# Kernel tuning notes

Measured on AMD Instinct MI355X. Metric: run time of the kernel, lower is better.

Reference implementation:

```python
import jax, jax.numpy as jnp
import numpy as np

N = 50000
E = 800000
F_IN = 512
H = 128
K = 10
ALPHA = 0.1
EPS = 1e-5  # BatchNorm eps


def setup_inputs() -> dict:
    key = jax.random.key(0)
    ks = jax.random.split(key, 16)
    x = jax.random.normal(ks[0], (N, F_IN), dtype=jnp.float32)
    edge_index = jax.random.randint(ks[1], (2, E), 0, N, dtype=jnp.int64)
    # Linear weights (xavier-ish scale)
    W1 = jax.random.normal(ks[2], (F_IN, H), dtype=jnp.float32) * (1.0 / np.sqrt(F_IN))
    b1 = jnp.zeros((H,), dtype=jnp.float32)
    W2 = jax.random.normal(ks[3], (H, H), dtype=jnp.float32) * (1.0 / np.sqrt(H))
    b2 = jnp.zeros((H,), dtype=jnp.float32)
    # BatchNorm (eval mode: running stats)
    gamma1 = jnp.ones((H,), dtype=jnp.float32)
    beta1 = jnp.zeros((H,), dtype=jnp.float32)
    mean1 = jax.random.normal(ks[4], (H,), dtype=jnp.float32) * 0.1
    var1 = jax.random.uniform(ks[5], (H,), dtype=jnp.float32) + 0.5
    gamma2 = jnp.ones((H,), dtype=jnp.float32)
    beta2 = jnp.zeros((H,), dtype=jnp.float32)
    mean2 = jax.random.normal(ks[6], (H,), dtype=jnp.float32) * 0.1
    var2 = jax.random.uniform(ks[7], (H,), dtype=jnp.float32) + 0.5
    return {
        "x": x, "edge_index": edge_index,
        "W1": W1, "b1": b1, "gamma1": gamma1, "beta1": beta1, "mean1": mean1, "var1": var1,
        "W2": W2, "b2": b2, "gamma2": gamma2, "beta2": beta2, "mean2": mean2, "var2": var2,
    }


def _bn_eval(h, gamma, beta, mean, var):
    return (h - mean) * jax.lax.rsqrt(var + EPS) * gamma + beta


def _appnp_prop(h, edge_index):
    # add self loops
    loop = jnp.arange(N, dtype=edge_index.dtype)
    src = jnp.concatenate([edge_index[0], loop])
    dst = jnp.concatenate([edge_index[1], loop])
    # symmetric GCN normalization: deg^{-1/2}[src] * deg^{-1/2}[dst]
    deg = jax.ops.segment_sum(jnp.ones_like(src, dtype=h.dtype), dst, num_segments=N)
    dinv = jax.lax.rsqrt(jnp.maximum(deg, 1.0))
    norm = dinv[src] * dinv[dst]  # [E+N]
    h0 = h

    def step(carry, _):
        msg = carry[src] * norm[:, None]                    # [E+N, H]
        agg = jax.ops.segment_sum(msg, dst, num_segments=N)  # [N, H]
        return (1.0 - ALPHA) * agg + ALPHA * h0, None

    out, _ = jax.lax.scan(step, h, None, length=K)
    return out


def reference(x, edge_index, W1, b1, gamma1, beta1, mean1, var1,
              W2, b2, gamma2, beta2, mean2, var2):
    h = jax.nn.relu(x @ W1 + b1)
    h = _bn_eval(h, gamma1, beta1, mean1, var1)
    # dropout inactive (eval mode)
    h = h @ W2 + b2
    h = _bn_eval(h, gamma2, beta2, mean2, var2)
    return _appnp_prop(h, edge_index)
```

## Files before the change

### kernel.cpp

```cpp
#include <hip/hip_runtime.h>

#define ALPHA_F 0.1f
#define EPS_F   1e-5f

typedef float    f32x4 __attribute__((ext_vector_type(4)));
typedef _Float16 h16x8 __attribute__((ext_vector_type(8)));
typedef _Float16 h16x2 __attribute__((ext_vector_type(2)));

__device__ __forceinline__ void gll16(const void* g, void* l)
{
    __builtin_amdgcn_global_load_lds(
        (const __attribute__((address_space(1))) void*)g,
        (__attribute__((address_space(3))) void*)l, 16, 0, 0);
}

__device__ __forceinline__ int pad_cnt(int d) { return (d + 8) & ~7; }

__device__ __forceinline__ unsigned pack_csr(int s, float w)
{
    _Float16 h = (_Float16)w;
    return (unsigned)(s & 0xFFFF)
         | ((unsigned)__builtin_bit_cast(unsigned short, h) << 16);
}

__global__ void convert_wstg(const float* __restrict__ W,
                             _Float16* __restrict__ Wstg, int K)
{
    int idx = blockIdx.x * 256 + threadIdx.x;
    if (idx < K * 128) {
        int k = idx >> 7, n = idx & 127;
        int i = k >> 5, kg = (k >> 3) & 3, j = k & 7;
        Wstg[(size_t)i * 4096 + (kg * 128 + n) * 8 + j] = (_Float16)W[idx];
    }
}

__global__ __launch_bounds__(256) void gemm_stage_bn_h(
    const _Float16* __restrict__ Ah,
    const _Float16* __restrict__ Wstg,
    const float* __restrict__ bias,
    const float* __restrict__ gamma, const float* __restrict__ beta,
    const float* __restrict__ mean,  const float* __restrict__ var,
    _Float16* __restrict__ outh, int M, int K)
{
    __shared__ __align__(16) char Abuf[2][8192];
    __shared__ __align__(16) char Wbuf[2][8192];

    const int t   = threadIdx.x;
    const int w   = t >> 6;
    const int l   = t & 63;
    const int l15 = l & 15;
    const int lk  = l >> 4;
    const int bm  = blockIdx.x * 64;
    const int nk  = K >> 5;
    const int row = w * 16 + l15;

    f32x4 acc[8];
#pragma unroll
    for (int f = 0; f < 8; ++f) acc[f] = (f32x4){0.f, 0.f, 0.f, 0.f};

    auto stage = [&](int buf, int i) {
        const char* wsrc = (const char*)Wstg + (size_t)i * 8192;
#pragma unroll
        for (int c = 0; c < 2; ++c) {
            const int base = w * 128 + c * 64;
            gll16(wsrc + (size_t)(base + l) * 16, &Wbuf[buf][base * 16]);
        }
        const int base = w * 64;
        const int sl   = base + l;
        const int r    = sl >> 2;
        const int ch   = (sl & 3) ^ (r & 3);
        int gr = bm + r; gr = (gr < M) ? gr : (M - 1);
        const char* src = (const char*)Ah + ((size_t)gr * K + i * 32) * 2
                          + (size_t)ch * 16;
        gll16(src, &Abuf[buf][base * 16]);
    };

    auto compute = [&](int buf) {
        h16x8 a = *(const h16x8*)&Abuf[buf][(row * 4 + (lk ^ (row & 3))) * 16];
#pragma unroll
        for (int f = 0; f < 8; ++f) {
            h16x8 b = *(const h16x8*)&Wbuf[buf][(lk * 128 + f * 16 + l15) * 16];
            acc[f] = __builtin_amdgcn_mfma_f32_16x16x32_f16(a, b, acc[f], 0, 0, 0);
        }
    };

    stage(0, 0);
    for (int i = 0; i < nk; ++i) {
        __syncthreads();
        if (i + 1 < nk) stage((i + 1) & 1, i + 1);
        compute(i & 1);
    }

#pragma unroll
    for (int f = 0; f < 8; ++f) {
        const int col = f * 16 + l15;
        float s  = gamma[col] * rsqrtf(var[col] + EPS_F);
        float sh = beta[col] - mean[col] * s;
        float bb = bias[col];
#pragma unroll
        for (int rr = 0; rr < 4; ++rr) {
            int rg = bm + w * 16 + lk * 4 + rr;
            if (rg < M)
                outh[(size_t)rg * 128 + col] =
                    (_Float16)((acc[f][rr] + bb) * s + sh);
        }
    }
}

__global__ __launch_bounds__(256) void fused_gemm1_scatter(
    const float* __restrict__ Af,
    const _Float16* __restrict__ Wstg,
    const float* __restrict__ bias,
    const float* __restrict__ gamma, const float* __restrict__ beta,
    const float* __restrict__ mean,  const float* __restrict__ var,
    _Float16* __restrict__ outh, int M, int K, int GB,
    const int* __restrict__ src, const int* __restrict__ dst, int E,
    const float* __restrict__ dinv, int* __restrict__ cursor,
    unsigned* __restrict__ csr4)
{
    __shared__ __align__(16) char Abuf[2][8192];
    __shared__ __align__(16) char Wbuf[2][8192];

    if (blockIdx.x >= GB) {
        int e = (blockIdx.x - GB) * 256 + threadIdx.x;
        if (e < E) {
            int s = src[e], d = dst[e];
            int pos = atomicAdd(&cursor[d], 1);
            csr4[pos] = pack_csr(s, dinv[s] * dinv[d]);
        }
        return;
    }

    const int t   = threadIdx.x;
    const int w   = t >> 6;
    const int l   = t & 63;
    const int l15 = l & 15;
    const int lk  = l >> 4;
    const int bm  = blockIdx.x * 64;
    const int nk  = K >> 5;
    const int row = w * 16 + l15;

    f32x4 acc[8];
#pragma unroll
    for (int f = 0; f < 8; ++f) acc[f] = (f32x4){0.f, 0.f, 0.f, 0.f};

    auto stage = [&](int buf, int i) {
        const char* wsrc = (const char*)Wstg + (size_t)i * 8192;
#pragma unroll
        for (int c = 0; c < 2; ++c) {
            const int base = w * 128 + c * 64;
            gll16(wsrc + (size_t)(base + l) * 16, &Wbuf[buf][base * 16]);
        }
#pragma unroll
        for (int c = 0; c < 2; ++c) {
            const int base = w * 128 + c * 64;
            const int sl   = base + l;
            const int r    = sl >> 3;
            const int ch   = (sl & 7) ^ (r & 7);
            int gr = bm + r; gr = (gr < M) ? gr : (M - 1);
            const char* srcp = (const char*)Af + ((size_t)gr * K + i * 32) * 4
                               + (size_t)ch * 16;
            gll16(srcp, &Abuf[buf][base * 16]);
        }
    };

    auto compute = [&](int buf) {
        f32x4 a0 = *(const f32x4*)&Abuf[buf][(row * 8 + ((2 * lk)     ^ (row & 7))) * 16];
        f32x4 a1 = *(const f32x4*)&Abuf[buf][(row * 8 + ((2 * lk + 1) ^ (row & 7))) * 16];
        h16x8 a;
#pragma unroll
        for (int j = 0; j < 4; ++j) {
            a[j]     = (_Float16)a0[j];
            a[4 + j] = (_Float16)a1[j];
        }
#pragma unroll
        for (int f = 0; f < 8; ++f) {
            h16x8 b = *(const h16x8*)&Wbuf[buf][(lk * 128 + f * 16 + l15) * 16];
            acc[f] = __builtin_amdgcn_mfma_f32_16x16x32_f16(a, b, acc[f], 0, 0, 0);
        }
    };

    stage(0, 0);
    for (int i = 0; i < nk; ++i) {
        __syncthreads();
        if (i + 1 < nk) stage((i + 1) & 1, i + 1);
        compute(i & 1);
    }

#pragma unroll
    for (int f = 0; f < 8; ++f) {
        const int col = f * 16 + l15;
        float s  = gamma[col] * rsqrtf(var[col] + EPS_F);
        float sh = beta[col] - mean[col] * s;
        float bb = bias[col];
#pragma unroll
        for (int rr = 0; rr < 4; ++rr) {
            int rg = bm + w * 16 + lk * 4 + rr;
            if (rg < M) {
                float v = fmaxf(acc[f][rr] + bb, 0.f);
                outh[(size_t)rg * 128 + col] = (_Float16)(v * s + sh);
            }
        }
    }
}

__global__ void count_deg(const int* __restrict__ dst, int E, int* __restrict__ deg)
{
    int e = blockIdx.x * 256 + threadIdx.x;
    if (e < E) atomicAdd(&deg[dst[e]], 1);
}

__global__ __launch_bounds__(256) void scan_block_sums(
    const int* __restrict__ deg, int* __restrict__ bsum, int N)
{
    __shared__ int sh[256];
    const int t  = threadIdx.x;
    const int i0 = blockIdx.x * 1024 + t * 4;
    int s = 0;
    if (i0 + 3 < N) {
        int4 d4 = *(const int4*)(deg + i0);
        s = pad_cnt(d4.x) + pad_cnt(d4.y) + pad_cnt(d4.z) + pad_cnt(d4.w);
    } else {
#pragma unroll
        for (int j = 0; j < 4; ++j)
            if (i0 + j < N) s += pad_cnt(deg[i0 + j]);
    }
    sh[t] = s;
    __syncthreads();
#pragma unroll
    for (int d = 128; d > 0; d >>= 1) {
        if (t < d) sh[t] += sh[t + d];
        __syncthreads();
    }
    if (t == 0) bsum[blockIdx.x] = sh[0];
}

__global__ __launch_bounds__(256) void scan_offsets(
    const int* __restrict__ deg, const int* __restrict__ bsum,
    int* __restrict__ offs, int* __restrict__ cursor,
    float* __restrict__ dinv, int N, int B)
{
    __shared__ int sh[256];
    __shared__ int sbase;
    const int b = blockIdx.x, t = threadIdx.x;

    int v = (t < b && t < B) ? bsum[t] : 0;
    sh[t] = v;
    __syncthreads();
#pragma unroll
    for (int d = 128; d > 0; d >>= 1) {
        if (t < d) sh[t] += sh[t + d];
        __syncthreads();
    }
    if (t == 0) sbase = sh[0];
    __syncthreads();

    const int i0 = b * 1024 + t * 4;
    int c[4], s = 0;
#pragma unroll
    for (int j = 0; j < 4; ++j) {
        int i = i0 + j;
        c[j] = (i < N) ? pad_cnt(deg[i]) : 0;
        s += c[j];
    }
    sh[t] = s;
    __syncthreads();
    for (int d = 1; d < 256; d <<= 1) {
        int o = (t >= d) ? sh[t - d] : 0;
        __syncthreads();
        sh[t] += o;
        __syncthreads();
    }
    int run = sbase + sh[t] - s;
#pragma unroll
    for (int j = 0; j < 4; ++j) {
        int i = i0 + j;
        if (i < N) {
            offs[i]   = run;
            cursor[i] = run;
            dinv[i]   = rsqrtf((float)(deg[i] + 1));
            run += c[j];
        }
    }
    if (b == B - 1 && t == 255) offs[N] = run;
}

__global__ void fill_self_pad(const int* __restrict__ offs, const int* __restrict__ deg,
                              const float* __restrict__ dinv,
                              unsigned* __restrict__ csr4, int N)
{
    int i = blockIdx.x * 256 + threadIdx.x;
    if (i < N) {
        int base = offs[i], d = deg[i], end = offs[i + 1];
        float di = dinv[i];
        csr4[base + d] = pack_csr(i, di * di);
        for (int p = base + d + 1; p < end; ++p)
            csr4[p] = pack_csr(i, 0.f);
    }
}

#define NWAVES 8192

__global__ __launch_bounds__(256) void appnp_step(
    const _Float16* __restrict__ cur, const _Float16* __restrict__ h0,
    const int* __restrict__ offs, const unsigned* __restrict__ csr4,
    _Float16* __restrict__ nxt, float* __restrict__ fout, int N)
{
    const int wv0  = __builtin_amdgcn_readfirstlane(
                        (int)((blockIdx.x * 256u + threadIdx.x) >> 6));
    const int lane = (int)(threadIdx.x & 63u);
    const int g    = lane >> 4;
    const int fl   = (lane & 15) * 8;

    for (int i = wv0; i < N; i += NWAVES) {
        int e   = offs[i];
        int end = offs[i + 1];

        h16x2 acc[4];
#pragma unroll
        for (int j = 0; j < 4; ++j) acc[j] = (h16x2){(_Float16)0, (_Float16)0};

        uint2 m = *(const uint2*)(csr4 + e + 2 * g);
        h16x8 vA = *(const h16x8*)(cur + (size_t)(m.x & 0xFFFFu) * 128 + fl);
        h16x8 vB = *(const h16x8*)(cur + (size_t)(m.y & 0xFFFFu) * 128 + fl);

        for (e += 8; e < end; e += 8) {
            uint2 m2 = *(const uint2*)(csr4 + e + 2 * g);
            h16x8 vA2 = *(const h16x8*)(cur + (size_t)(m2.x & 0xFFFFu) * 128 + fl);
            h16x8 vB2 = *(const h16x8*)(cur + (size_t)(m2.y & 0xFFFFu) * 128 + fl);
            _Float16 ha = __builtin_bit_cast(_Float16, (unsigned short)(m.x >> 16));
            _Float16 hb = __builtin_bit_cast(_Float16, (unsigned short)(m.y >> 16));
            h16x2 wa = (h16x2){ha, ha}, wb = (h16x2){hb, hb};
#pragma unroll
            for (int j = 0; j < 4; ++j) {
                h16x2 va = (h16x2){vA[2 * j], vA[2 * j + 1]};
                h16x2 vb = (h16x2){vB[2 * j], vB[2 * j + 1]};
                acc[j] = __builtin_elementwise_fma(wa, va, acc[j]);
                acc[j] = __builtin_elementwise_fma(wb, vb, acc[j]);
            }
            m = m2; vA = vA2; vB = vB2;
        }
        {
            _Float16 ha = __builtin_bit_cast(_Float16, (unsigned short)(m.x >> 16));
            _Float16 hb = __builtin_bit_cast(_Float16, (unsigned short)(m.y >> 16));
            h16x2 wa = (h16x2){ha, ha}, wb = (h16x2){hb, hb};
#pragma unroll
            for (int j = 0; j < 4; ++j) {
                h16x2 va = (h16x2){vA[2 * j], vA[2 * j + 1]};
                h16x2 vb = (h16x2){vB[2 * j], vB[2 * j + 1]};
                acc[j] = __builtin_elementwise_fma(wa, va, acc[j]);
                acc[j] = __builtin_elementwise_fma(wb, vb, acc[j]);
            }
        }

        float o[8];
#pragma unroll
        for (int j = 0; j < 4; ++j) {
            o[2 * j]     = (float)acc[j][0];
            o[2 * j + 1] = (float)acc[j][1];
        }
#pragma unroll
        for (int j = 0; j < 8; ++j) {
            o[j] += __shfl_xor(o[j], 16);
            o[j] += __shfl_xor(o[j], 32);
        }

        if (lane < 16) {
            h16x8 hv = *(const h16x8*)(h0 + (size_t)i * 128 + fl);
#pragma unroll
            for (int j = 0; j < 8; ++j)
                o[j] = ALPHA_F * (float)hv[j] + (1.f - ALPHA_F) * o[j];
            if (fout) {
                f32x4 o0, o1;
#pragma unroll
                for (int j = 0; j < 4; ++j) { o0[j] = o[j]; o1[j] = o[4 + j]; }
                *(f32x4*)(fout + (size_t)i * 128 + fl)     = o0;
                *(f32x4*)(fout + (size_t)i * 128 + fl + 4) = o1;
            } else {
                h16x8 o16;
#pragma unroll
                for (int j = 0; j < 8; ++j) o16[j] = (_Float16)o[j];
                *(h16x8*)(nxt + (size_t)i * 128 + fl) = o16;
            }
        }
    }
}

static inline size_t align_up(size_t x) { return (x + 255) & ~(size_t)255; }

extern "C" void kernel_launch(void* const* d_in, const int* in_sizes, int n_in,
                              void* d_out, int out_size, void* d_ws, size_t ws_size,
                              hipStream_t stream)
{
    const float* x   = (const float*)d_in[0];
    const int*   ei  = (const int*)d_in[1];
    const float* W1  = (const float*)d_in[2];
    const float* b1  = (const float*)d_in[3];
    const float* g1  = (const float*)d_in[4];
    const float* be1 = (const float*)d_in[5];
    const float* m1  = (const float*)d_in[6];
    const float* v1  = (const float*)d_in[7];
    const float* W2  = (const float*)d_in[8];
    const float* b2  = (const float*)d_in[9];
    const float* g2  = (const float*)d_in[10];
    const float* be2 = (const float*)d_in[11];
    const float* m2  = (const float*)d_in[12];
    const float* v2  = (const float*)d_in[13];

    const int N = in_sizes[0] / 512;
    const int E = in_sizes[1] / 2;
    const int* src = ei;
    const int* dst = ei + E;
    const int CSR_CAP = E + 8 * N;
    const int NB = (N + 1023) / 1024;
    const int GB = (N + 63) / 64;
    const int SB = (E + 255) / 256;

    char* ws = (char*)d_ws;
    size_t off = 0;
    _Float16* hAh = (_Float16*)(ws + off); off += align_up((size_t)N * 128 * 2);
    _Float16* h0h = (_Float16*)(ws + off); off += align_up((size_t)N * 128 * 2);
    _Float16* p0  = (_Float16*)(ws + off); off += align_up((size_t)N * 128 * 2);
    _Float16* p1  = (_Float16*)(ws + off); off += align_up((size_t)N * 128 * 2);
    int*    deg  = (int*)(ws + off);    off += align_up((size_t)N * 4);
    float*  dinv = (float*)(ws + off);  off += align_up((size_t)N * 4);
    int*    offs = (int*)(ws + off);    off += align_up((size_t)(N + 1) * 4);
    int*    curs = (int*)(ws + off);    off += align_up((size_t)N * 4);
    int*    bsum = (int*)(ws + off);    off += align_up((size_t)256 * 4);
    unsigned* csr4 = (unsigned*)(ws + off); off += align_up((size_t)CSR_CAP * 4);
    _Float16* w1s = (_Float16*)(ws + off); off += align_up((size_t)512 * 128 * 2);
    _Float16* w2s = (_Float16*)(ws + off); off += align_up((size_t)128 * 128 * 2);

    hipMemsetAsync(deg, 0, (size_t)N * 4, stream);
    count_deg<<<(E + 255) / 256, 256, 0, stream>>>(dst, E, deg);
    scan_block_sums<<<NB, 256, 0, stream>>>(deg, bsum, N);
    scan_offsets<<<NB, 256, 0, stream>>>(deg, bsum, offs, curs, dinv, N, NB);

    convert_wstg<<<(512 * 128 + 255) / 256, 256, 0, stream>>>(W1, w1s, 512);
    convert_wstg<<<(128 * 128 + 255) / 256, 256, 0, stream>>>(W2, w2s, 128);

    fused_gemm1_scatter<<<GB + SB, 256, 0, stream>>>(
        x, w1s, b1, g1, be1, m1, v1, hAh, N, 512, GB,
        src, dst, E, dinv, curs, csr4);

    fill_self_pad<<<(N + 255) / 256, 256, 0, stream>>>(offs, deg, dinv, csr4, N);
    gemm_stage_bn_h<<<GB, 256, 0, stream>>>(
        hAh, w2s, b2, g2, be2, m2, v2, h0h, N, 128);

    const _Float16* cur = h0h;
    for (int k = 0; k < 10; ++k) {
        _Float16* nxt = (k & 1) ? p1 : p0;
        float* fo = (k == 9) ? (float*)d_out : nullptr;
        appnp_step<<<NWAVES / 4, 256, 0, stream>>>(
            cur, h0h, offs, csr4, nxt, fo, N);
        cur = nxt;
    }

    (void)n_in; (void)out_size; (void)ws_size;
}
```

Baseline: 405.0 us.

## Partition degree counting and CSR scatter atomics by XCD destination range

The degree-count kernel and the edge-scatter half of the fused GEMM kernel now use a fixed grid of chunked blocks. The chunks are replicated across the 8 XCDs, chosen by blockIdx & 7. Each block scans a strided slice of the edges and handles only those whose destination falls in its XCD's eighth of the node range. The aim is to keep each destination's atomic counters and CSR writes within a single XCD's L2, avoiding cross-die atomic traffic and contention. In exchange, every edge's dst index is now read 8 times.

```diff
diff --git a/kernel.cpp b/kernel.cpp
--- a/kernel.cpp
+++ b/kernel.cpp
@@ -113,8 +113,8 @@
     const float* __restrict__ bias,
     const float* __restrict__ gamma, const float* __restrict__ beta,
     const float* __restrict__ mean,  const float* __restrict__ var,
-    _Float16* __restrict__ outh, int M, int K, int GB,
-    const int* __restrict__ src, const int* __restrict__ dst, int E,
+    _Float16* __restrict__ outh, int M, int K, int GB, int N,
+    const int* __restrict__ src, const int* __restrict__ dst, int E, int SC,
     const float* __restrict__ dinv, int* __restrict__ cursor,
     unsigned* __restrict__ csr4)
 {
@@ -122,11 +122,18 @@
     __shared__ __align__(16) char Wbuf[2][8192];
 
     if (blockIdx.x >= GB) {
-        int e = (blockIdx.x - GB) * 256 + threadIdx.x;
-        if (e < E) {
-            int s = src[e], d = dst[e];
-            int pos = atomicAdd(&cursor[d], 1);
-            csr4[pos] = pack_csr(s, dinv[s] * dinv[d]);
+        const int xcd  = (int)(blockIdx.x & 7);
+        const int nper = (N + 7) >> 3;
+        const int lo   = xcd * nper;
+        const int hi   = min(lo + nper, N);
+        const int cid  = (int)(blockIdx.x - GB) >> 3;
+        for (int e = cid * 256 + (int)threadIdx.x; e < E; e += SC * 256) {
+            int d = dst[e];
+            if (d >= lo && d < hi) {
+                int s = src[e];
+                int pos = atomicAdd(&cursor[d], 1);
+                csr4[pos] = pack_csr(s, dinv[s] * dinv[d]);
+            }
         }
         return;
     }
@@ -204,10 +211,20 @@
     }
 }
 
-__global__ void count_deg(const int* __restrict__ dst, int E, int* __restrict__ deg)
-{
-    int e = blockIdx.x * 256 + threadIdx.x;
-    if (e < E) atomicAdd(&deg[dst[e]], 1);
+#define DEG_CHUNKS 256
+
+__global__ void count_deg(const int* __restrict__ dst, int E,
+                          int* __restrict__ deg, int N)
+{
+    const int xcd  = (int)(blockIdx.x & 7);
+    const int nper = (N + 7) >> 3;
+    const int lo   = xcd * nper;
+    const int hi   = min(lo + nper, N);
+    const int cid  = (int)(blockIdx.x >> 3);
+    for (int e = cid * 256 + (int)threadIdx.x; e < E; e += DEG_CHUNKS * 256) {
+        int d = dst[e];
+        if (d >= lo && d < hi) atomicAdd(&deg[d], 1);
+    }
 }
 
 __global__ __launch_bounds__(256) void scan_block_sums(
@@ -414,7 +431,7 @@
     const int CSR_CAP = E + 8 * N;
     const int NB = (N + 1023) / 1024;
     const int GB = (N + 63) / 64;
-    const int SB = (E + 255) / 256;
+    const int SC = 1024;
 
     char* ws = (char*)d_ws;
     size_t off = 0;
@@ -432,16 +449,16 @@
     _Float16* w2s = (_Float16*)(ws + off); off += align_up((size_t)128 * 128 * 2);
 
     hipMemsetAsync(deg, 0, (size_t)N * 4, stream);
-    count_deg<<<(E + 255) / 256, 256, 0, stream>>>(dst, E, deg);
+    count_deg<<<8 * DEG_CHUNKS, 256, 0, stream>>>(dst, E, deg, N);
     scan_block_sums<<<NB, 256, 0, stream>>>(deg, bsum, N);
     scan_offsets<<<NB, 256, 0, stream>>>(deg, bsum, offs, curs, dinv, N, NB);
 
     convert_wstg<<<(512 * 128 + 255) / 256, 256, 0, stream>>>(W1, w1s, 512);
     convert_wstg<<<(128 * 128 + 255) / 256, 256, 0, stream>>>(W2, w2s, 128);
 
-    fused_gemm1_scatter<<<GB + SB, 256, 0, stream>>>(
-        x, w1s, b1, g1, be1, m1, v1, hAh, N, 512, GB,
-        src, dst, E, dinv, curs, csr4);
+    fused_gemm1_scatter<<<GB + 8 * SC, 256, 0, stream>>>(
+        x, w1s, b1, g1, be1, m1, v1, hAh, N, 512, GB, N,
+        src, dst, E, SC, dinv, curs, csr4);
 
     fill_self_pad<<<(N + 255) / 256, 256, 0, stream>>>(offs, deg, dinv, csr4, N);
     gemm_stage_bn_h<<<GB, 256, 0, stream>>>(
```

New measurement: 417.9 us. 1.03x slower.
